# Performance work log

Hardware: AMD Instinct MI355X
Metric: run time of the kernel (lower is better)

The kernel has to match this reference:

```python
import jax, jax.numpy as jnp
import numpy as np

C_IN = 64
C_QK = C_IN // 8  # 8
B, H, W = 8, 64, 64


def setup_inputs() -> dict:
    key = jax.random.key(0)
    ks = jax.random.split(key, 8)
    s_in = 1.0 / np.sqrt(C_IN)
    return {
        "x": jax.random.normal(ks[0], (B, C_IN, H, W), dtype=jnp.float32),
        "Wf": jax.random.normal(ks[1], (C_QK, C_IN), dtype=jnp.float32) * s_in,
        "bf": jax.random.normal(ks[2], (C_QK,), dtype=jnp.float32) * 0.01,
        "Wg": jax.random.normal(ks[3], (C_QK, C_IN), dtype=jnp.float32) * s_in,
        "bg": jax.random.normal(ks[4], (C_QK,), dtype=jnp.float32) * 0.01,
        "Wh": jax.random.normal(ks[5], (C_IN, C_IN), dtype=jnp.float32) * s_in,
        "bh": jax.random.normal(ks[6], (C_IN,), dtype=jnp.float32) * 0.01,
        "gamma": jax.random.normal(ks[7], (1,), dtype=jnp.float32) * 0.1,
    }


def reference(x, Wf, bf, Wg, bg, Wh, bh, gamma):
    Bn, C, Hn, Wn = x.shape
    N = Hn * Wn
    xf = x.reshape(Bn, C, N)  # (B, C, HW)
    # 1x1 convs == per-pixel linear projections
    fx = jnp.einsum('bcn,oc->bno', xf, Wf) + bf            # (B, HW, C/8)  (permuted query)
    gx = jnp.einsum('bcn,oc->bon', xf, Wg) + bg[:, None]   # (B, C/8, HW)
    hx = jnp.einsum('bcn,oc->bon', xf, Wh) + bh[:, None]   # (B, C,  HW)
    s_mtx = jnp.einsum('bno,bom->bnm', fx, gx)             # (B, HW, HW)
    attention = jax.nn.softmax(s_mtx, axis=-2)             # softmax over dim=-2 (rows)
    o = jnp.einsum('bcn,bnm->bcm', hx, attention)          # (B, C, HW)
    return x + gamma * o.reshape(Bn, C, Hn, Wn)
```

## Files before the change

### kernel.cpp

```cpp
#include <hip/hip_runtime.h>
#include <hip/hip_bf16.h>
#include <math.h>

#define CIN 64
#define CQK 8
#define BATCH 8
#define NPOS 4096
#define TN 128
#define NT (NPOS / TN)

typedef __attribute__((ext_vector_type(8))) short s16x8;
typedef __attribute__((ext_vector_type(4))) float f32x4;
typedef __attribute__((ext_vector_type(16))) float f32x16;

#define Z16 {0,0,0,0,0,0,0,0,0,0,0,0,0,0,0,0}

__device__ inline unsigned cvt_pk_bf16(float lo, float hi) {
    unsigned r;
    asm("v_cvt_pk_bf16_f32 %0, %1, %2" : "=v"(r) : "v"(lo), "v"(hi));
    return r;
}

__global__ __launch_bounds__(256) void proj_kernel(
    const float* __restrict__ x,
    const float* __restrict__ Wf, const float* __restrict__ bf,
    const float* __restrict__ Wg, const float* __restrict__ bg,
    const float* __restrict__ Wh, const float* __restrict__ bh,
    unsigned short* __restrict__ Kp, unsigned short* __restrict__ Qp,
    unsigned short* __restrict__ Vimg)
{
    __shared__ float xs[CIN * 66];
    __shared__ float bss[80];

    const int tid = threadIdx.x;
    const int b   = blockIdx.y;
    const int n0  = blockIdx.x * 64;

    if (tid < 80)
        bss[tid] = (tid < 8) ? bf[tid] : (tid < 16) ? bg[tid - 8] : bh[tid - 16];

    {
        const int c   = tid >> 2;
        const int seg = tid & 3;
        const float* src = x + ((size_t)(b * CIN + c)) * NPOS + n0 + seg * 16;
        float* dst = xs + c * 66 + seg * 16;
#pragma unroll
        for (int k = 0; k < 4; ++k) {
            const float4 v = *(const float4*)(src + k * 4);
            *(float2*)(dst + k * 4)     = make_float2(v.x, v.y);
            *(float2*)(dst + k * 4 + 2) = make_float2(v.z, v.w);
        }
    }

    const int l  = tid & 63;
    const int w  = tid >> 6;
    const int lm = l & 15;
    const int h  = l >> 4;

    auto wfrag = [&](const float* Wrow) -> s16x8 {
        const float4 a  = *(const float4*)(Wrow);
        const float4 bq = *(const float4*)(Wrow + 4);
        union { unsigned u[4]; s16x8 v; } r;
        r.u[0] = cvt_pk_bf16(a.x, a.y);
        r.u[1] = cvt_pk_bf16(a.z, a.w);
        r.u[2] = cvt_pk_bf16(bq.x, bq.y);
        r.u[3] = cvt_pk_bf16(bq.z, bq.w);
        return r.v;
    };

    const float* kqrow = (lm < 8) ? (Wf + lm * CIN) : (Wg + (lm - 8) * CIN);
    const s16x8 wkq0 = wfrag(kqrow + h * 8);
    const s16x8 wkq1 = wfrag(kqrow + h * 8 + 32);
    s16x8 wv0[4], wv1[4];
#pragma unroll
    for (int vt = 0; vt < 4; ++vt) {
        const float* vr = Wh + (vt * 16 + lm) * CIN + h * 8;
        wv0[vt] = wfrag(vr);
        wv1[vt] = wfrag(vr + 32);
    }

    __syncthreads();

    union { unsigned u[4]; s16x8 v; } xf0, xf1;
#pragma unroll
    for (int e2 = 0; e2 < 4; ++e2) {
        const int c = h * 8 + e2 * 2;
        xf0.u[e2] = cvt_pk_bf16(xs[c * 66 + w * 16 + lm],
                                xs[(c + 1) * 66 + w * 16 + lm]);
        xf1.u[e2] = cvt_pk_bf16(xs[(c + 32) * 66 + w * 16 + lm],
                                xs[(c + 33) * 66 + w * 16 + lm]);
    }

    const f32x4 z = {0.f, 0.f, 0.f, 0.f};
    f32x4 kq = __builtin_amdgcn_mfma_f32_16x16x32_bf16(wkq0, xf0.v, z, 0, 0, 0);
    kq = __builtin_amdgcn_mfma_f32_16x16x32_bf16(wkq1, xf1.v, kq, 0, 0, 0);
    f32x4 va[4];
#pragma unroll
    for (int vt = 0; vt < 4; ++vt) {
        va[vt] = __builtin_amdgcn_mfma_f32_16x16x32_bf16(xf0.v, wv0[vt], z, 0, 0, 0);
        va[vt] = __builtin_amdgcn_mfma_f32_16x16x32_bf16(xf1.v, wv1[vt], va[vt], 0, 0, 0);
    }

    const float LOG2E = 1.44269504088896f;

    {
        const int n = n0 + w * 16 + lm;
        float v0 = kq[0] + bss[h * 4 + 0];
        float v1 = kq[1] + bss[h * 4 + 1];
        float v2 = kq[2] + bss[h * 4 + 2];
        float v3 = kq[3] + bss[h * 4 + 3];
        if (h >= 2) { v0 *= LOG2E; v1 *= LOG2E; v2 *= LOG2E; v3 *= LOG2E; }
        uint2 pk;
        pk.x = cvt_pk_bf16(v0, v1);
        pk.y = cvt_pk_bf16(v2, v3);
        unsigned short* dstq =
            (h < 2 ? Kp : Qp) + ((size_t)(b * NPOS + n)) * CQK + (h & 1) * 4;
        *(uint2*)dstq = pk;
    }

    {
        const int t128 = n0 >> 7;
        const int sub  = ((n0 & 127) >> 5) + (w >> 1);
        unsigned short* dstB =
            Vimg + ((size_t)(b * 32 + t128)) * 8192 + (size_t)sub * 2048;
        const int jj   = (h & 1) * 2 + (w & 1);
        const int half = h >> 1;
#pragma unroll
        for (int vt = 0; vt < 4; ++vt) {
            const int C = vt * 16 + lm;
            const float bb = bss[16 + C];
            uint2 pk;
            pk.x = cvt_pk_bf16(va[vt][0] + bb, va[vt][1] + bb);
            pk.y = cvt_pk_bf16(va[vt][2] + bb, va[vt][3] + bb);
            const int p = ((jj & 1) * 2 + (C >> 5)) * 64 + (jj >> 1) * 32 + (C & 31);
            *(uint2*)(dstB + p * 8 + half * 4) = pk;
        }
    }
}

__global__ __launch_bounds__(256, 2) void attn_kernel(
    const unsigned short* __restrict__ Kp, const unsigned short* __restrict__ Qp,
    const unsigned short* __restrict__ Vimg, const float* __restrict__ x,
    const float* __restrict__ gamma, float* __restrict__ out)
{
    __shared__ __align__(16) float smem[4 * 64 * 36 + 128];
    float* reg = smem;
    float* rsl = smem + 4 * 64 * 36;

    const int tid = threadIdx.x;
    const int l   = tid & 63;
    const int w   = tid >> 6;
    const int lc  = l & 31;
    const int h   = l >> 5;
    const int id  = blockIdx.x;
    const int b   = id & 7;
    const int m0  = (id >> 3) * 64;

    const unsigned short* Kbat = Kp + (size_t)b * NPOS * CQK;
    const char* Vbat = (const char*)(Vimg + (size_t)b * NPOS * CIN);

    s16x8 qf0 = {0,0,0,0,0,0,0,0}, qf1 = {0,0,0,0,0,0,0,0};
    if (h == 0) {
        qf0 = *(const s16x8*)(Qp + ((size_t)(b * NPOS + m0 + lc)) * CQK);
        qf1 = *(const s16x8*)(Qp + ((size_t)(b * NPOS + m0 + 32 + lc)) * CQK);
    }

    f32x16 acc00 = Z16, acc01 = Z16, acc10 = Z16, acc11 = Z16;
    f32x16 rs0 = Z16, rs1 = Z16;
    const s16x8 vones = {0x3F80, 0x3F80, 0x3F80, 0x3F80,
                         0x3F80, 0x3F80, 0x3F80, 0x3F80};

    s16x8 vfA[4], vfB[4], kaA, kaB;

    auto loadV = [&](s16x8* vf, int t) {
        const char* base = Vbat + (size_t)t * 16384 + w * 4096 + l * 16;
#pragma unroll
        for (int c = 0; c < 4; ++c)
            vf[c] = *(const s16x8*)(base + c * 1024);
    };
    auto loadK = [&](s16x8& kr, int t) {
        kr = *(const s16x8*)(Kbat + ((size_t)(t * TN + w * 32 + lc)) * CQK);
    };

    auto compute = [&](const s16x8& ka, const s16x8* vf) {
        __builtin_amdgcn_s_setprio(1);
        const f32x16 z = Z16;
        f32x16 sc0 = __builtin_amdgcn_mfma_f32_32x32x16_bf16(ka, qf0, z, 0, 0, 0);
        f32x16 sc1 = __builtin_amdgcn_mfma_f32_32x32x16_bf16(ka, qf1, z, 0, 0, 0);
        float p0[16], p1[16];
#pragma unroll
        for (int rr = 0; rr < 16; ++rr) {
            p0[rr] = __builtin_amdgcn_exp2f(sc0[rr]);
            p1[rr] = __builtin_amdgcn_exp2f(sc1[rr]);
        }
        union { unsigned u[4]; s16x8 v; } A10, A20, A11, A21;
#pragma unroll
        for (int i = 0; i < 4; ++i) {
            A10.u[i] = cvt_pk_bf16(p0[2 * i], p0[2 * i + 1]);
            A20.u[i] = cvt_pk_bf16(p0[8 + 2 * i], p0[9 + 2 * i]);
            A11.u[i] = cvt_pk_bf16(p1[2 * i], p1[2 * i + 1]);
            A21.u[i] = cvt_pk_bf16(p1[8 + 2 * i], p1[9 + 2 * i]);
        }
        rs0 = __builtin_amdgcn_mfma_f32_32x32x16_bf16(A10.v, vones, rs0, 0, 0, 0);
        rs0 = __builtin_amdgcn_mfma_f32_32x32x16_bf16(A20.v, vones, rs0, 0, 0, 0);
        rs1 = __builtin_amdgcn_mfma_f32_32x32x16_bf16(A11.v, vones, rs1, 0, 0, 0);
        rs1 = __builtin_amdgcn_mfma_f32_32x32x16_bf16(A21.v, vones, rs1, 0, 0, 0);
        acc00 = __builtin_amdgcn_mfma_f32_32x32x16_bf16(A10.v, vf[0], acc00, 0, 0, 0);
        acc00 = __builtin_amdgcn_mfma_f32_32x32x16_bf16(A20.v, vf[2], acc00, 0, 0, 0);
        acc01 = __builtin_amdgcn_mfma_f32_32x32x16_bf16(A10.v, vf[1], acc01, 0, 0, 0);
        acc01 = __builtin_amdgcn_mfma_f32_32x32x16_bf16(A20.v, vf[3], acc01, 0, 0, 0);
        acc10 = __builtin_amdgcn_mfma_f32_32x32x16_bf16(A11.v, vf[0], acc10, 0, 0, 0);
        acc10 = __builtin_amdgcn_mfma_f32_32x32x16_bf16(A21.v, vf[2], acc10, 0, 0, 0);
        acc11 = __builtin_amdgcn_mfma_f32_32x32x16_bf16(A11.v, vf[1], acc11, 0, 0, 0);
        acc11 = __builtin_amdgcn_mfma_f32_32x32x16_bf16(A21.v, vf[3], acc11, 0, 0, 0);
        __builtin_amdgcn_s_setprio(0);
    };

    loadV(vfA, 0); loadK(kaA, 0);
    loadV(vfB, 1); loadK(kaB, 1);

#pragma unroll 1
    for (int t = 0; t < NT; t += 2) {
        asm volatile("s_waitcnt vmcnt(5)" ::: "memory");
        compute(kaA, vfA);
        if (t + 2 < NT) {
            loadV(vfA, t + 2); loadK(kaA, t + 2);
            asm volatile("s_waitcnt vmcnt(5)" ::: "memory");
        } else {
            asm volatile("s_waitcnt vmcnt(0)" ::: "memory");
        }
        compute(kaB, vfB);
        if (t + 3 < NT) { loadV(vfB, t + 3); loadK(kaB, t + 3); }
    }

    const float gm = gamma[0];
    auto epi = [&](const f32x16& a0, const f32x16& a1, const f32x16& rsv,
                   int mOff) {
#pragma unroll
        for (int rq = 0; rq < 4; ++rq) {
            const int mb = 8 * rq + 4 * h;
            const f32x4 q0 = {a0[4 * rq], a0[4 * rq + 1], a0[4 * rq + 2], a0[4 * rq + 3]};
            const f32x4 q1 = {a1[4 * rq], a1[4 * rq + 1], a1[4 * rq + 2], a1[4 * rq + 3]};
            *(f32x4*)(reg + w * 2304 + lc * 36 + mb)        = q0;
            *(f32x4*)(reg + w * 2304 + (32 + lc) * 36 + mb) = q1;
            if (lc == 0) {
                const f32x4 qr = {rsv[4 * rq], rsv[4 * rq + 1], rsv[4 * rq + 2], rsv[4 * rq + 3]};
                *(f32x4*)(rsl + w * 32 + mb) = qr;
            }
        }
        __syncthreads();
        const int c  = tid >> 2;
        const int mq = tid & 3;
        const size_t base = ((size_t)(b * CIN + c)) * NPOS + m0 + mOff + mq * 8;
#pragma unroll
        for (int q4 = 0; q4 < 2; ++q4) {
            const float4 xv = *(const float4*)(x + base + q4 * 4);
            float4 o;
#pragma unroll
            for (int i = 0; i < 4; ++i) {
                const int ml = mq * 8 + q4 * 4 + i;
                const float rsum = (rsl[ml] + rsl[32 + ml]) + (rsl[64 + ml] + rsl[96 + ml]);
                const int oi = c * 36 + ml;
                const float os = (reg[oi] + reg[2304 + oi]) + (reg[4608 + oi] + reg[6912 + oi]);
                ((float*)&o)[i] = ((const float*)&xv)[i] + gm * os / rsum;
            }
            *(float4*)(out + base + q4 * 4) = o;
        }
        __syncthreads();
    };
    epi(acc00, acc01, rs0, 0);
    epi(acc10, acc11, rs1, 32);
}

extern "C" void kernel_launch(void* const* d_in, const int* in_sizes, int n_in,
                              void* d_out, int out_size, void* d_ws, size_t ws_size,
                              hipStream_t stream) {
    const float* x     = (const float*)d_in[0];
    const float* Wf    = (const float*)d_in[1];
    const float* bf    = (const float*)d_in[2];
    const float* Wg    = (const float*)d_in[3];
    const float* bg    = (const float*)d_in[4];
    const float* Wh    = (const float*)d_in[5];
    const float* bh    = (const float*)d_in[6];
    const float* gamma = (const float*)d_in[7];
    float* out = (float*)d_out;

    unsigned short* Kp = (unsigned short*)d_ws;
    unsigned short* Qp = Kp + (size_t)BATCH * NPOS * CQK;
    unsigned short* Vimg = Qp + (size_t)BATCH * NPOS * CQK;

    dim3 pgrid(NPOS / 64, BATCH);
    proj_kernel<<<pgrid, 256, 0, stream>>>(x, Wf, bf, Wg, bg, Wh, bh, Kp, Qp, Vimg);

    attn_kernel<<<dim3(BATCH * NPOS / 64), 256, 0, stream>>>(Kp, Qp, Vimg, x, gamma, out);
}
```

Before: 43.40 us.

## Software-pipeline score MFMAs one tile ahead and compute row sums with VALU

Restructures the attention main loop so the QK score MFMAs for the next tile are issued before the exp/PV work of the current tile, with K loads reordered ahead of V loads and waitcnt thresholds adjusted. Replaces the ones-vector MFMAs that computed softmax denominators with scalar VALU adds plus a cross-half shuffle, writing per-wave row sums to shared memory. The aim is to hide MFMA-to-exp dependency latency and remove four MFMAs per tile. In exchange it holds extra score accumulators in registers, which adds register pressure at two waves per SIMD, and it puts more adds on the VALU.

```diff
diff --git a/kernel.cpp b/kernel.cpp
--- a/kernel.cpp
+++ b/kernel.cpp
@@ -143,7 +143,7 @@
     const unsigned short* __restrict__ Vimg, const float* __restrict__ x,
     const float* __restrict__ gamma, float* __restrict__ out)
 {
-    __shared__ __align__(16) float smem[4 * 64 * 36 + 128];
+    __shared__ __align__(16) float smem[4 * 64 * 36 + 256];
     float* reg = smem;
     float* rsl = smem + 4 * 64 * 36;
 
@@ -166,11 +166,11 @@
     }
 
     f32x16 acc00 = Z16, acc01 = Z16, acc10 = Z16, acc11 = Z16;
-    f32x16 rs0 = Z16, rs1 = Z16;
-    const s16x8 vones = {0x3F80, 0x3F80, 0x3F80, 0x3F80,
-                         0x3F80, 0x3F80, 0x3F80, 0x3F80};
+    float rsum0 = 0.f, rsum1 = 0.f;
 
     s16x8 vfA[4], vfB[4], kaA, kaB;
+    f32x16 scA0, scA1, scB0, scB1;
+    const f32x16 z = Z16;
 
     auto loadV = [&](s16x8* vf, int t) {
         const char* base = Vbat + (size_t)t * 16384 + w * 4096 + l * 16;
@@ -182,60 +182,80 @@
         kr = *(const s16x8*)(Kbat + ((size_t)(t * TN + w * 32 + lc)) * CQK);
     };
 
-    auto compute = [&](const s16x8& ka, const s16x8* vf) {
+    auto proc = [&](f32x16& s0, f32x16& s1, const s16x8* vf) {
         __builtin_amdgcn_s_setprio(1);
-        const f32x16 z = Z16;
-        f32x16 sc0 = __builtin_amdgcn_mfma_f32_32x32x16_bf16(ka, qf0, z, 0, 0, 0);
-        f32x16 sc1 = __builtin_amdgcn_mfma_f32_32x32x16_bf16(ka, qf1, z, 0, 0, 0);
-        float p0[16], p1[16];
-#pragma unroll
-        for (int rr = 0; rr < 16; ++rr) {
-            p0[rr] = __builtin_amdgcn_exp2f(sc0[rr]);
-            p1[rr] = __builtin_amdgcn_exp2f(sc1[rr]);
-        }
-        union { unsigned u[4]; s16x8 v; } A10, A20, A11, A21;
+#pragma unroll
+        for (int rr = 0; rr < 16; ++rr) s0[rr] = __builtin_amdgcn_exp2f(s0[rr]);
+        union { unsigned u[4]; s16x8 v; } A1, A2;
 #pragma unroll
         for (int i = 0; i < 4; ++i) {
-            A10.u[i] = cvt_pk_bf16(p0[2 * i], p0[2 * i + 1]);
-            A20.u[i] = cvt_pk_bf16(p0[8 + 2 * i], p0[9 + 2 * i]);
-            A11.u[i] = cvt_pk_bf16(p1[2 * i], p1[2 * i + 1]);
-            A21.u[i] = cvt_pk_bf16(p1[8 + 2 * i], p1[9 + 2 * i]);
-        }
-        rs0 = __builtin_amdgcn_mfma_f32_32x32x16_bf16(A10.v, vones, rs0, 0, 0, 0);
-        rs0 = __builtin_amdgcn_mfma_f32_32x32x16_bf16(A20.v, vones, rs0, 0, 0, 0);
-        rs1 = __builtin_amdgcn_mfma_f32_32x32x16_bf16(A11.v, vones, rs1, 0, 0, 0);
-        rs1 = __builtin_amdgcn_mfma_f32_32x32x16_bf16(A21.v, vones, rs1, 0, 0, 0);
-        acc00 = __builtin_amdgcn_mfma_f32_32x32x16_bf16(A10.v, vf[0], acc00, 0, 0, 0);
-        acc00 = __builtin_amdgcn_mfma_f32_32x32x16_bf16(A20.v, vf[2], acc00, 0, 0, 0);
-        acc01 = __builtin_amdgcn_mfma_f32_32x32x16_bf16(A10.v, vf[1], acc01, 0, 0, 0);
-        acc01 = __builtin_amdgcn_mfma_f32_32x32x16_bf16(A20.v, vf[3], acc01, 0, 0, 0);
-        acc10 = __builtin_amdgcn_mfma_f32_32x32x16_bf16(A11.v, vf[0], acc10, 0, 0, 0);
-        acc10 = __builtin_amdgcn_mfma_f32_32x32x16_bf16(A21.v, vf[2], acc10, 0, 0, 0);
-        acc11 = __builtin_amdgcn_mfma_f32_32x32x16_bf16(A11.v, vf[1], acc11, 0, 0, 0);
-        acc11 = __builtin_amdgcn_mfma_f32_32x32x16_bf16(A21.v, vf[3], acc11, 0, 0, 0);
+            A1.u[i] = cvt_pk_bf16(s0[2 * i], s0[2 * i + 1]);
+            A2.u[i] = cvt_pk_bf16(s0[8 + 2 * i], s0[9 + 2 * i]);
+        }
+        rsum0 += (((s0[0] + s0[1]) + (s0[2] + s0[3])) +
+                  ((s0[4] + s0[5]) + (s0[6] + s0[7]))) +
+                 (((s0[8] + s0[9]) + (s0[10] + s0[11])) +
+                  ((s0[12] + s0[13]) + (s0[14] + s0[15])));
+        acc00 = __builtin_amdgcn_mfma_f32_32x32x16_bf16(A1.v, vf[0], acc00, 0, 0, 0);
+        acc00 = __builtin_amdgcn_mfma_f32_32x32x16_bf16(A2.v, vf[2], acc00, 0, 0, 0);
+        acc01 = __builtin_amdgcn_mfma_f32_32x32x16_bf16(A1.v, vf[1], acc01, 0, 0, 0);
+        acc01 = __builtin_amdgcn_mfma_f32_32x32x16_bf16(A2.v, vf[3], acc01, 0, 0, 0);
+#pragma unroll
+        for (int rr = 0; rr < 16; ++rr) s1[rr] = __builtin_amdgcn_exp2f(s1[rr]);
+        union { unsigned u[4]; s16x8 v; } B1, B2;
+#pragma unroll
+        for (int i = 0; i < 4; ++i) {
+            B1.u[i] = cvt_pk_bf16(s1[2 * i], s1[2 * i + 1]);
+            B2.u[i] = cvt_pk_bf16(s1[8 + 2 * i], s1[9 + 2 * i]);
+        }
+        rsum1 += (((s1[0] + s1[1]) + (s1[2] + s1[3])) +
+                  ((s1[4] + s1[5]) + (s1[6] + s1[7]))) +
+                 (((s1[8] + s1[9]) + (s1[10] + s1[11])) +
+                  ((s1[12] + s1[13]) + (s1[14] + s1[15])));
+        acc10 = __builtin_amdgcn_mfma_f32_32x32x16_bf16(B1.v, vf[0], acc10, 0, 0, 0);
+        acc10 = __builtin_amdgcn_mfma_f32_32x32x16_bf16(B2.v, vf[2], acc10, 0, 0, 0);
+        acc11 = __builtin_amdgcn_mfma_f32_32x32x16_bf16(B1.v, vf[1], acc11, 0, 0, 0);
+        acc11 = __builtin_amdgcn_mfma_f32_32x32x16_bf16(B2.v, vf[3], acc11, 0, 0, 0);
         __builtin_amdgcn_s_setprio(0);
     };
 
-    loadV(vfA, 0); loadK(kaA, 0);
-    loadV(vfB, 1); loadK(kaB, 1);
+    loadK(kaA, 0); loadV(vfA, 0);
+    loadK(kaB, 1); loadV(vfB, 1);
+    asm volatile("s_waitcnt vmcnt(5)" ::: "memory");
+    scA0 = __builtin_amdgcn_mfma_f32_32x32x16_bf16(kaA, qf0, z, 0, 0, 0);
+    scA1 = __builtin_amdgcn_mfma_f32_32x32x16_bf16(kaA, qf1, z, 0, 0, 0);
 
 #pragma unroll 1
-    for (int t = 0; t < NT; t += 2) {
-        asm volatile("s_waitcnt vmcnt(5)" ::: "memory");
-        compute(kaA, vfA);
-        if (t + 2 < NT) {
-            loadV(vfA, t + 2); loadK(kaA, t + 2);
-            asm volatile("s_waitcnt vmcnt(5)" ::: "memory");
-        } else {
-            asm volatile("s_waitcnt vmcnt(0)" ::: "memory");
-        }
-        compute(kaB, vfB);
-        if (t + 3 < NT) { loadV(vfB, t + 3); loadK(kaB, t + 3); }
+    for (int t = 0; t < NT - 2; t += 2) {
+        asm volatile("s_waitcnt vmcnt(4)" ::: "memory");
+        scB0 = __builtin_amdgcn_mfma_f32_32x32x16_bf16(kaB, qf0, z, 0, 0, 0);
+        scB1 = __builtin_amdgcn_mfma_f32_32x32x16_bf16(kaB, qf1, z, 0, 0, 0);
+        loadK(kaA, t + 2);
+        proc(scA0, scA1, vfA);
+        loadV(vfA, t + 2);
+        asm volatile("s_waitcnt vmcnt(4)" ::: "memory");
+        scA0 = __builtin_amdgcn_mfma_f32_32x32x16_bf16(kaA, qf0, z, 0, 0, 0);
+        scA1 = __builtin_amdgcn_mfma_f32_32x32x16_bf16(kaA, qf1, z, 0, 0, 0);
+        loadK(kaB, t + 3);
+        proc(scB0, scB1, vfB);
+        loadV(vfB, t + 3);
+    }
+    asm volatile("s_waitcnt vmcnt(4)" ::: "memory");
+    scB0 = __builtin_amdgcn_mfma_f32_32x32x16_bf16(kaB, qf0, z, 0, 0, 0);
+    scB1 = __builtin_amdgcn_mfma_f32_32x32x16_bf16(kaB, qf1, z, 0, 0, 0);
+    proc(scA0, scA1, vfA);
+    asm volatile("s_waitcnt vmcnt(0)" ::: "memory");
+    proc(scB0, scB1, vfB);
+
+    rsum0 += __shfl_xor(rsum0, 32, 64);
+    rsum1 += __shfl_xor(rsum1, 32, 64);
+    if (h == 0) {
+        rsl[w * 64 + lc]      = rsum0;
+        rsl[w * 64 + 32 + lc] = rsum1;
     }
 
     const float gm = gamma[0];
-    auto epi = [&](const f32x16& a0, const f32x16& a1, const f32x16& rsv,
-                   int mOff) {
+    auto epi = [&](const f32x16& a0, const f32x16& a1, int mOff) {
 #pragma unroll
         for (int rq = 0; rq < 4; ++rq) {
             const int mb = 8 * rq + 4 * h;
@@ -243,10 +263,6 @@
             const f32x4 q1 = {a1[4 * rq], a1[4 * rq + 1], a1[4 * rq + 2], a1[4 * rq + 3]};
             *(f32x4*)(reg + w * 2304 + lc * 36 + mb)        = q0;
             *(f32x4*)(reg + w * 2304 + (32 + lc) * 36 + mb) = q1;
-            if (lc == 0) {
-                const f32x4 qr = {rsv[4 * rq], rsv[4 * rq + 1], rsv[4 * rq + 2], rsv[4 * rq + 3]};
-                *(f32x4*)(rsl + w * 32 + mb) = qr;
-            }
         }
         __syncthreads();
         const int c  = tid >> 2;
@@ -259,7 +275,8 @@
 #pragma unroll
             for (int i = 0; i < 4; ++i) {
                 const int ml = mq * 8 + q4 * 4 + i;
-                const float rsum = (rsl[ml] + rsl[32 + ml]) + (rsl[64 + ml] + rsl[96 + ml]);
+                const float rsum = (rsl[mOff + ml] + rsl[64 + mOff + ml]) +
+                                   (rsl[128 + mOff + ml] + rsl[192 + mOff + ml]);
                 const int oi = c * 36 + ml;
                 const float os = (reg[oi] + reg[2304 + oi]) + (reg[4608 + oi] + reg[6912 + oi]);
                 ((float*)&o)[i] = ((const float*)&xv)[i] + gm * os / rsum;
@@ -268,8 +285,8 @@
         }
         __syncthreads();
     };
-    epi(acc00, acc01, rs0, 0);
-    epi(acc10, acc11, rs1, 32);
+    epi(acc00, acc01, 0);
+    epi(acc10, acc11, 32);
 }
 
 extern "C" void kernel_launch(void* const* d_in, const int* in_sizes, int n_in,
```

Result: faster. 40.21 us (-7.4%).
